# Optimization experiments

Measured on AMD Instinct MI355X. Metric: run time of the kernel, lower is better.

Reference implementation:

```python
import jax, jax.numpy as jnp
import numpy as np
from jax import lax

C = 16  # channels

def _conv1x1(x, w, b):
    # 1x1x1 Conv3d == channel-mixing einsum. x: [B,C,T,H,W], w: [O,C], b: [O]
    return jnp.einsum('oc,bcthw->bothw', w, x) + b[None, :, None, None, None]

def _ffn(x, w1, b1, w2, b2):
    return _conv1x1(jnp.tanh(_conv1x1(x, w1, b1)), w2, b2)

def setup_inputs() -> dict:
    key = jax.random.key(0)
    ks = jax.random.split(key, 12)
    s = 0.1
    x = jax.random.normal(ks[0], (2, C, 31, 256, 256), dtype=jnp.float32)
    mk_w = lambda k: jax.random.normal(k, (C, C), dtype=jnp.float32) * s
    mk_b = lambda k: jax.random.normal(k, (C,), dtype=jnp.float32) * s
    return {
        'x': x,
        'wf1': mk_w(ks[1]), 'bf1': mk_b(ks[2]),
        'wf2': mk_w(ks[3]), 'bf2': mk_b(ks[4]),
        'ww1': mk_w(ks[5]), 'bw1': mk_b(ks[6]),
        'ww2': mk_w(ks[7]), 'bw2': mk_b(ks[8]),
        'wsca': mk_w(ks[9]), 'bsca': mk_b(ks[10]),
    }

def reference(x, wf1, bf1, wf2, bf2, ww1, bw1, ww2, bw2, wsca, bsca):
    # Gates from two 1x1-conv FFNs
    Z = jnp.tanh(_ffn(x, wf1, bf1, wf2, bf2))          # [B,C,T,H,W]
    Fg = jax.nn.sigmoid(_ffn(x, ww1, bw1, ww2, bw2))   # [B,C,T,H,W]
    # Linear recurrence over time dim: h_t = f_t * h_{t-1} + (1-f_t) * z_t, h_{-1}=0
    Zt = jnp.moveaxis(Z, 2, 0)   # [T,B,C,H,W]
    Ft = jnp.moveaxis(Fg, 2, 0)
    def step(h, zf):
        z, f = zf
        h = f * h + (1.0 - f) * z
        return h, h
    h0 = jnp.zeros_like(Zt[0])
    _, hs = lax.scan(step, h0, (Zt, Ft))
    out = jnp.moveaxis(hs, 0, 2)  # [B,C,T,H,W]
    # Simplified channel attention: global avg pool -> 1x1 conv -> sigmoid -> scale
    gap = jnp.mean(out, axis=(2, 3, 4), keepdims=True)  # [B,C,1,1,1]
    att = jax.nn.sigmoid(_conv1x1(gap, wsca, bsca))
    return att * out
```

## Files before the change

### kernel.cpp

```cpp
#include <hip/hip_runtime.h>
#include <hip/hip_bf16.h>

#define TDIM 31
#define TS   65536
#define CS   (TDIM * TS)
#define BS   (16 * CS)
#define NTOT (2 * BS)
#define K1_BLOCKS 8192
#define GAP_INV (1.0f / (31.0f * 65536.0f))

typedef __attribute__((ext_vector_type(8))) short short8v;
typedef __attribute__((ext_vector_type(4))) float f32x4;
typedef __attribute__((ext_vector_type(8))) unsigned short ushort8v;

__device__ __forceinline__ float frcp(float v){ return __builtin_amdgcn_rcpf(v); }
__device__ __forceinline__ float fexp2_(float v){ return __builtin_amdgcn_exp2f(v); }
__device__ __forceinline__ float ftanh(float x){ float e = fexp2_(x*2.8853900817779268f); return 1.0f - 2.0f*frcp(e+1.0f); }
__device__ __forceinline__ float fsigm(float x){ float e = fexp2_(x*-1.4426950408889634f); return frcp(1.0f+e); }
__device__ __forceinline__ unsigned rhu16(float x){ return (__float_as_uint(x) + 0x8000u) >> 16; }
__device__ __forceinline__ float bf2f(unsigned b){ return __uint_as_float(b << 16); }
__device__ __forceinline__ unsigned pkhi(unsigned u0, unsigned u1){ return __builtin_amdgcn_perm(u1, u0, 0x07060302u); }

template<bool BF16H>
__global__ __launch_bounds__(256, 4) void k1_fused(
    const float* __restrict__ x,
    const float* __restrict__ wf1, const float* __restrict__ bf1,
    const float* __restrict__ wf2, const float* __restrict__ bf2,
    const float* __restrict__ ww1, const float* __restrict__ bw1,
    const float* __restrict__ ww2, const float* __restrict__ bw2,
    float* __restrict__ out, unsigned short* __restrict__ hb,
    float* __restrict__ partials)
{
    __shared__ unsigned int sGate[TDIM][16][16];
    __shared__ alignas(16) char sAfaw[4][1024];

    const int tid  = threadIdx.x;
    const int lane = tid & 63;
    const int wv   = tid >> 6;
    const int col  = lane & 15;
    const int kg   = lane >> 4;
    const bool lok = (kg >= 2);
    const int blk  = blockIdx.x;
    const int b    = blk >> 12;
    const int p0   = (blk & 4095) << 4;

    short8v A1f, A2f, A1w, A2w, Af2, Aw2;
    {
        const int c0 = (kg & 1) * 8;
#pragma unroll
        for (int i = 0; i < 8; ++i) {
            const float w1 = wf1[col*16 + c0 + i];
            unsigned u1 = __float_as_uint(w1);
            float lo1 = w1 - __uint_as_float(u1 & 0xFFFF0000u);
            A1f[i] = (short)(u1 >> 16);
            A2f[i] = (short)(__float_as_uint(lo1) >> 16);
            const float w2 = ww1[col*16 + c0 + i];
            unsigned u2 = __float_as_uint(w2);
            float lo2 = w2 - __uint_as_float(u2 & 0xFFFF0000u);
            A1w[i] = (short)(u2 >> 16);
            A2w[i] = (short)(__float_as_uint(lo2) >> 16);
            const float v2f = wf2[col*16 + c0 + i];
            const float v2w = ww2[col*16 + c0 + i];
            Af2[i] = (kg < 2)  ? (short)rhu16(v2f) : (short)0;
            Aw2[i] = (kg >= 2) ? (short)rhu16(v2w) : (short)0;
        }
    }
    f32x4 b1fv, b1wv, b2fv, b2wv;
#pragma unroll
    for (int r = 0; r < 4; ++r) {
        b1fv[r] = bf1[kg*4+r]; b1wv[r] = bw1[kg*4+r];
        b2fv[r] = bf2[kg*4+r]; b2wv[r] = bw2[kg*4+r];
    }

    auto process = [&](int u, const float* xv) {
        unsigned H[4], L[4];
#pragma unroll
        for (int j = 0; j < 4; ++j) {
            const unsigned u0 = __float_as_uint(xv[2*j]);
            const unsigned u1 = __float_as_uint(xv[2*j+1]);
            const float l0 = xv[2*j]   - __uint_as_float(u0 & 0xFFFF0000u);
            const float l1 = xv[2*j+1] - __uint_as_float(u1 & 0xFFFF0000u);
            H[j] = pkhi(u0, u1);
            L[j] = pkhi(__float_as_uint(l0), __float_as_uint(l1));
        }
        uint4 bxu;
        bxu.x = lok ? L[0] : H[0]; bxu.y = lok ? L[1] : H[1];
        bxu.z = lok ? L[2] : H[2]; bxu.w = lok ? L[3] : H[3];
        const short8v bx = __builtin_bit_cast(short8v, bxu);

        f32x4 accf = b1fv, accw = b1wv;
        accf = __builtin_amdgcn_mfma_f32_16x16x32_bf16(A1f, bx, accf, 0, 0, 0);
        accf = __builtin_amdgcn_mfma_f32_16x16x32_bf16(A2f, bx, accf, 0, 0, 0);
        accw = __builtin_amdgcn_mfma_f32_16x16x32_bf16(A1w, bx, accw, 0, 0, 0);
        accw = __builtin_amdgcn_mfma_f32_16x16x32_bf16(A2w, bx, accw, 0, 0, 0);

        const float a0 = ftanh(accf[0]), a1 = ftanh(accf[1]);
        const float a2 = ftanh(accf[2]), a3 = ftanh(accf[3]);
        const float w0 = ftanh(accw[0]), w1 = ftanh(accw[1]);
        const float w2 = ftanh(accw[2]), w3 = ftanh(accw[3]);
        char* base = sAfaw[wv] + col * 64;
        *(uint2*)(base + kg*8)      = make_uint2((rhu16(a1)<<16)|rhu16(a0), (rhu16(a3)<<16)|rhu16(a2));
        *(uint2*)(base + 32 + kg*8) = make_uint2((rhu16(w1)<<16)|rhu16(w0), (rhu16(w3)<<16)|rhu16(w2));
        const short8v b2 = *(const short8v*)(base + ((kg & 1) * 16 + (kg >> 1) * 32));
        f32x4 acz = b2fv, acw = b2wv;
        acz = __builtin_amdgcn_mfma_f32_16x16x32_bf16(Af2, b2, acz, 0, 0, 0);
        acw = __builtin_amdgcn_mfma_f32_16x16x32_bf16(Aw2, b2, acw, 0, 0, 0);

        unsigned w_[4];
#pragma unroll
        for (int r = 0; r < 4; ++r) {
            const float z = ftanh(acz[r]);
            const float f = fsigm(acw[r]);
            const int   zi = (int)__builtin_rintf(z * 32767.0f);
            const unsigned fu = (unsigned)(f * 65535.0f + 0.5f);
            w_[r] = ((unsigned)zi << 16) | (fu & 0xFFFFu);
        }
        *(uint4*)&sGate[u][col][kg*4] = make_uint4(w_[0], w_[1], w_[2], w_[3]);
    };

    const unsigned xbase = (unsigned)b * BS + (unsigned)p0 + (unsigned)col
                         + (unsigned)((kg & 1) * 8) * CS;
#define LOADU(dst, u_) { const float* xp = x + (size_t)xbase + (size_t)(u_) * TS; \
    _Pragma("unroll") for (int i = 0; i < 8; ++i) (dst)[i] = xp[i * CS]; }

    float xs0[8], xs1[8], xs2[8], xs3[8];
    LOADU(xs0, wv)
    LOADU(xs1, wv + 4)
    LOADU(xs2, wv + 8)
#pragma unroll
    for (int k = 0; k < 8; ++k) {
        const int u  = wv + 4 * k;
        const int uf = u + 12;
        switch (k & 3) {
            case 0: if (uf < TDIM) LOADU(xs3, uf) if (u < TDIM) process(u, xs0); break;
            case 1: if (uf < TDIM) LOADU(xs0, uf) if (u < TDIM) process(u, xs1); break;
            case 2: if (uf < TDIM) LOADU(xs1, uf) if (u < TDIM) process(u, xs2); break;
            default:if (uf < TDIM) LOADU(xs2, uf) if (u < TDIM) process(u, xs3); break;
        }
    }
#undef LOADU
    __syncthreads();

    if (tid < 64) {
        const int cg = tid >> 4, p = tid & 15;
        const unsigned obase = (unsigned)b * BS + (unsigned)p0 + (unsigned)p;
        float h[4] = {0.f,0.f,0.f,0.f}, s[4] = {0.f,0.f,0.f,0.f};
#pragma unroll 1
        for (int t = 0; t < TDIM; ++t) {
            const uint4 w4 = *(const uint4*)&sGate[t][p][cg*4];
#pragma unroll
            for (int j = 0; j < 4; ++j) {
                const int w = (int)(j==0 ? w4.x : j==1 ? w4.y : j==2 ? w4.z : w4.w);
                const float z = (float)(w >> 16) * (1.0f / 32767.0f);
                const float f = (float)(w & 0xFFFF) * (1.0f / 65535.0f);
                h[j] = fmaf(f, h[j] - z, z);
                s[j] += h[j];
                const unsigned oidx = obase + (unsigned)(cg*4+j) * CS + (unsigned)t * TS;
                if (BF16H) hb[oidx] = (unsigned short)rhu16(h[j]);
                else       out[oidx] = h[j];
            }
        }
#pragma unroll
        for (int j = 0; j < 4; ++j) {
#pragma unroll
            for (int off = 8; off; off >>= 1) s[j] += __shfl_down(s[j], off, 16);
        }
        if (p == 0) {
#pragma unroll
            for (int j = 0; j < 4; ++j) partials[blk * 16 + cg*4 + j] = s[j];
        }
    }
}

__global__ __launch_bounds__(1024) void k2_attention(
    const float* __restrict__ partials, const float* __restrict__ wsca,
    const float* __restrict__ bsca, float* __restrict__ att)
{
    __shared__ float red[2][16][32];
    __shared__ float gap[2][16];
    const int tid = threadIdx.x;
    {
        const int b = tid >> 9, c = (tid >> 5) & 15, seg = tid & 31;
        float s = 0.f;
        const float* p = partials + (size_t)(b * 4096 + seg * 128) * 16 + c;
        for (int j = 0; j < 128; ++j) s += p[j * 16];
        red[b][c][seg] = s;
    }
    __syncthreads();
    if (tid < 32) {
        const int b = tid >> 4, c = tid & 15;
        float s = 0.f;
#pragma unroll
        for (int g = 0; g < 32; ++g) s += red[b][c][g];
        gap[b][c] = s * GAP_INV;
    }
    __syncthreads();
    if (tid < 32) {
        const int b = tid >> 4, o = tid & 15;
        float acc = bsca[o];
#pragma unroll
        for (int c = 0; c < 16; ++c) acc = fmaf(wsca[o*16 + c], gap[b][c], acc);
        att[b*16 + o] = fsigm(acc);
    }
}

__global__ __launch_bounds__(1024) void k3_scale_b(
    const unsigned short* __restrict__ hb, const float* __restrict__ att,
    float* __restrict__ out)
{
    const int bc = blockIdx.y;
    const float a = att[bc];
    const unsigned i = blockIdx.x * 1024 + threadIdx.x;
    const size_t base = (size_t)bc * CS;
    const ushort8v v = ((const ushort8v*)(hb + base))[i];
    float4 o1, o2;
    o1.x = bf2f(v[0])*a; o1.y = bf2f(v[1])*a; o1.z = bf2f(v[2])*a; o1.w = bf2f(v[3])*a;
    o2.x = bf2f(v[4])*a; o2.y = bf2f(v[5])*a; o2.z = bf2f(v[6])*a; o2.w = bf2f(v[7])*a;
    float4* op = (float4*)(out + base);
    op[i*2]     = o1;
    op[i*2 + 1] = o2;
}

__global__ __launch_bounds__(1024) void k3_scale_a(
    const float* __restrict__ att, float* __restrict__ out)
{
    const int bc = blockIdx.y;
    const float a = att[bc];
    const unsigned i = blockIdx.x * 1024 + threadIdx.x;
    float4* op = (float4*)(out + (size_t)bc * CS);
    float4 v1 = op[i*2], v2 = op[i*2 + 1];
    v1.x *= a; v1.y *= a; v1.z *= a; v1.w *= a;
    v2.x *= a; v2.y *= a; v2.z *= a; v2.w *= a;
    op[i*2] = v1; op[i*2 + 1] = v2;
}

extern "C" void kernel_launch(void* const* d_in, const int* in_sizes, int n_in,
                              void* d_out, int out_size, void* d_ws, size_t ws_size,
                              hipStream_t stream) {
    const float* x    = (const float*)d_in[0];
    const float* wf1  = (const float*)d_in[1];
    const float* bf1  = (const float*)d_in[2];
    const float* wf2  = (const float*)d_in[3];
    const float* bf2  = (const float*)d_in[4];
    const float* ww1  = (const float*)d_in[5];
    const float* bw1  = (const float*)d_in[6];
    const float* ww2  = (const float*)d_in[7];
    const float* bw2  = (const float*)d_in[8];
    const float* wsca = (const float*)d_in[9];
    const float* bsca = (const float*)d_in[10];
    float* out = (float*)d_out;

    const size_t hbBytes   = (size_t)NTOT * 2;
    const size_t partBytes = (size_t)K1_BLOCKS * 16 * 4;
    const bool bf16h = ws_size >= hbBytes + partBytes + 256;

    unsigned short* hb = (unsigned short*)d_ws;
    float* partials = bf16h ? (float*)((char*)d_ws + hbBytes) : (float*)d_ws;
    float* att = partials + K1_BLOCKS * 16;

    if (bf16h) {
        k1_fused<true><<<K1_BLOCKS, 256, 0, stream>>>(x, wf1, bf1, wf2, bf2,
            ww1, bw1, ww2, bw2, out, hb, partials);
        k2_attention<<<1, 1024, 0, stream>>>(partials, wsca, bsca, att);
        k3_scale_b<<<dim3(248, 32), 1024, 0, stream>>>(hb, att, out);
    } else {
        k1_fused<false><<<K1_BLOCKS, 256, 0, stream>>>(x, wf1, bf1, wf2, bf2,
            ww1, bw1, ww2, bw2, out, hb, partials);
        k2_attention<<<1, 1024, 0, stream>>>(partials, wsca, bsca, att);
        k3_scale_a<<<dim3(248, 32), 1024, 0, stream>>>(att, out);
    }
}
```

Baseline: 352.4 us.

## Parallelize scan across all threads, swap LDS staging for shuffles, shrink prefetch depth

The time recurrence now runs on all 256 threads (one channel-pixel pair each) instead of only the first 64 threads handling four channels each. The gate buffer uses a swizzled layout so those reads avoid bank conflicts. The per-wave LDS staging buffer for the second MFMA's B operand is replaced by cross-lane shuffles, and the prefetch ring drops from four to three register buffers. Together these cut register and LDS use so occupancy can rise to 5 waves per SIMD, at the cost of more shuffle instructions and a shallower load pipeline.

Result: slower. 483.7 us (+37.3%).

```diff
diff --git a/kernel.cpp b/kernel.cpp
--- a/kernel.cpp
+++ b/kernel.cpp
@@ -22,7 +22,7 @@
 __device__ __forceinline__ unsigned pkhi(unsigned u0, unsigned u1){ return __builtin_amdgcn_perm(u1, u0, 0x07060302u); }
 
 template<bool BF16H>
-__global__ __launch_bounds__(256, 4) void k1_fused(
+__global__ __launch_bounds__(256, 5) void k1_fused(
     const float* __restrict__ x,
     const float* __restrict__ wf1, const float* __restrict__ bf1,
     const float* __restrict__ wf2, const float* __restrict__ bf2,
@@ -31,8 +31,7 @@
     float* __restrict__ out, unsigned short* __restrict__ hb,
     float* __restrict__ partials)
 {
-    __shared__ unsigned int sGate[TDIM][16][16];
-    __shared__ alignas(16) char sAfaw[4][1024];
+    __shared__ unsigned int sGate[TDIM * 256];
 
     const int tid  = threadIdx.x;
     const int lane = tid & 63;
@@ -72,6 +71,8 @@
         b2fv[r] = bf2[kg*4+r]; b2wv[r] = bw2[kg*4+r];
     }
 
+    const int lsrc = col + ((kg & 1) << 5);
+
     auto process = [&](int u, const float* xv) {
         unsigned H[4], L[4];
 #pragma unroll
@@ -98,24 +99,40 @@
         const float a2 = ftanh(accf[2]), a3 = ftanh(accf[3]);
         const float w0 = ftanh(accw[0]), w1 = ftanh(accw[1]);
         const float w2 = ftanh(accw[2]), w3 = ftanh(accw[3]);
-        char* base = sAfaw[wv] + col * 64;
-        *(uint2*)(base + kg*8)      = make_uint2((rhu16(a1)<<16)|rhu16(a0), (rhu16(a3)<<16)|rhu16(a2));
-        *(uint2*)(base + 32 + kg*8) = make_uint2((rhu16(w1)<<16)|rhu16(w0), (rhu16(w3)<<16)|rhu16(w2));
-        const short8v b2 = *(const short8v*)(base + ((kg & 1) * 16 + (kg >> 1) * 32));
+        const unsigned afP0 = (rhu16(a1) << 16) | rhu16(a0);
+        const unsigned afP1 = (rhu16(a3) << 16) | rhu16(a2);
+        const unsigned awP0 = (rhu16(w1) << 16) | rhu16(w0);
+        const unsigned awP1 = (rhu16(w3) << 16) | rhu16(w2);
+
+        const unsigned x0l = __shfl(afP0, lsrc, 64);
+        const unsigned x1l = __shfl(afP1, lsrc, 64);
+        const unsigned x0h = __shfl(afP0, lsrc + 16, 64);
+        const unsigned x1h = __shfl(afP1, lsrc + 16, 64);
+        const unsigned y0l = __shfl(awP0, lsrc, 64);
+        const unsigned y1l = __shfl(awP1, lsrc, 64);
+        const unsigned y0h = __shfl(awP0, lsrc + 16, 64);
+        const unsigned y1h = __shfl(awP1, lsrc + 16, 64);
+        uint4 b2u;
+        b2u.x = lok ? y0l : x0l;
+        b2u.y = lok ? y1l : x1l;
+        b2u.z = lok ? y0h : x0h;
+        b2u.w = lok ? y1h : x1h;
+        const short8v b2 = __builtin_bit_cast(short8v, b2u);
+
         f32x4 acz = b2fv, acw = b2wv;
         acz = __builtin_amdgcn_mfma_f32_16x16x32_bf16(Af2, b2, acz, 0, 0, 0);
         acw = __builtin_amdgcn_mfma_f32_16x16x32_bf16(Aw2, b2, acw, 0, 0, 0);
 
-        unsigned w_[4];
 #pragma unroll
         for (int r = 0; r < 4; ++r) {
             const float z = ftanh(acz[r]);
             const float f = fsigm(acw[r]);
             const int   zi = (int)__builtin_rintf(z * 32767.0f);
             const unsigned fu = (unsigned)(f * 65535.0f + 0.5f);
-            w_[r] = ((unsigned)zi << 16) | (fu & 0xFFFFu);
-        }
-        *(uint4*)&sGate[u][col][kg*4] = make_uint4(w_[0], w_[1], w_[2], w_[3]);
+            const unsigned wd = ((unsigned)zi << 16) | (fu & 0xFFFFu);
+            sGate[u*256 + r*64 + (kg>>1)*32 + (((r ^ kg) & 1) << 4)
+                  + ((col + 4*r) & 15)] = wd;
+        }
     };
 
     const unsigned xbase = (unsigned)b * BS + (unsigned)p0 + (unsigned)col
@@ -123,52 +140,47 @@
 #define LOADU(dst, u_) { const float* xp = x + (size_t)xbase + (size_t)(u_) * TS; \
     _Pragma("unroll") for (int i = 0; i < 8; ++i) (dst)[i] = xp[i * CS]; }
 
-    float xs0[8], xs1[8], xs2[8], xs3[8];
+    float xs0[8], xs1[8], xs2[8];
     LOADU(xs0, wv)
     LOADU(xs1, wv + 4)
-    LOADU(xs2, wv + 8)
 #pragma unroll
     for (int k = 0; k < 8; ++k) {
         const int u  = wv + 4 * k;
-        const int uf = u + 12;
-        switch (k & 3) {
-            case 0: if (uf < TDIM) LOADU(xs3, uf) if (u < TDIM) process(u, xs0); break;
-            case 1: if (uf < TDIM) LOADU(xs0, uf) if (u < TDIM) process(u, xs1); break;
-            case 2: if (uf < TDIM) LOADU(xs1, uf) if (u < TDIM) process(u, xs2); break;
-            default:if (uf < TDIM) LOADU(xs2, uf) if (u < TDIM) process(u, xs3); break;
+        const int uf = u + 8;
+        if ((k % 3) == 0) {
+            if (uf < TDIM) LOADU(xs2, uf)
+            if (u  < TDIM) process(u, xs0);
+        } else if ((k % 3) == 1) {
+            if (uf < TDIM) LOADU(xs0, uf)
+            if (u  < TDIM) process(u, xs1);
+        } else {
+            if (uf < TDIM) LOADU(xs1, uf)
+            if (u  < TDIM) process(u, xs2);
         }
     }
 #undef LOADU
     __syncthreads();
 
-    if (tid < 64) {
-        const int cg = tid >> 4, p = tid & 15;
-        const unsigned obase = (unsigned)b * BS + (unsigned)p0 + (unsigned)p;
-        float h[4] = {0.f,0.f,0.f,0.f}, s[4] = {0.f,0.f,0.f,0.f};
+    {
+        const int c = tid >> 4, p = tid & 15;
+        const unsigned base2 = (unsigned)((c & 3) * 64 + ((c >> 3) & 1) * 32
+                             + (((c ^ (c >> 2)) & 1) << 4) + ((p + 4 * c) & 15));
+        const unsigned obase = (unsigned)b * BS + (unsigned)c * CS
+                             + (unsigned)p0 + (unsigned)p;
+        float h = 0.f, s = 0.f;
 #pragma unroll 1
         for (int t = 0; t < TDIM; ++t) {
-            const uint4 w4 = *(const uint4*)&sGate[t][p][cg*4];
-#pragma unroll
-            for (int j = 0; j < 4; ++j) {
-                const int w = (int)(j==0 ? w4.x : j==1 ? w4.y : j==2 ? w4.z : w4.w);
-                const float z = (float)(w >> 16) * (1.0f / 32767.0f);
-                const float f = (float)(w & 0xFFFF) * (1.0f / 65535.0f);
-                h[j] = fmaf(f, h[j] - z, z);
-                s[j] += h[j];
-                const unsigned oidx = obase + (unsigned)(cg*4+j) * CS + (unsigned)t * TS;
-                if (BF16H) hb[oidx] = (unsigned short)rhu16(h[j]);
-                else       out[oidx] = h[j];
-            }
-        }
-#pragma unroll
-        for (int j = 0; j < 4; ++j) {
-#pragma unroll
-            for (int off = 8; off; off >>= 1) s[j] += __shfl_down(s[j], off, 16);
-        }
-        if (p == 0) {
-#pragma unroll
-            for (int j = 0; j < 4; ++j) partials[blk * 16 + cg*4 + j] = s[j];
-        }
+            const unsigned wd = sGate[t * 256 + base2];
+            const float z = (float)((int)wd >> 16) * (1.0f / 32767.0f);
+            const float f = (float)(wd & 0xFFFFu) * (1.0f / 65535.0f);
+            h = fmaf(f, h - z, z);
+            s += h;
+            if (BF16H) hb[obase + (unsigned)t * TS] = (unsigned short)rhu16(h);
+            else       out[obase + (unsigned)t * TS] = h;
+        }
+#pragma unroll
+        for (int off = 8; off; off >>= 1) s += __shfl_down(s, off, 16);
+        if (p == 0) partials[blk * 16 + c] = s;
     }
 }
 
```
